# Kernel optimization log

Measured on AMD Instinct MI355X. Metric: run time of the kernel, lower is better.

## Reference

```python
import jax, jax.numpy as jnp
import numpy as np

D_MODEL = 512
NUM_HEADS = 8
D_K = D_MODEL // NUM_HEADS


def setup_inputs() -> dict:
    key = jax.random.key(0)
    k0, k1, k2, k3, k4 = jax.random.split(key, 5)
    s = 1.0 / np.sqrt(D_MODEL)
    return {
        "x": jax.random.normal(k0, (2, 4096, D_MODEL), dtype=jnp.float32),
        "W_q": jax.random.normal(k1, (D_MODEL, D_MODEL), dtype=jnp.float32) * s,
        "W_k": jax.random.normal(k2, (D_MODEL, D_MODEL), dtype=jnp.float32) * s,
        "W_v": jax.random.normal(k3, (D_MODEL, D_MODEL), dtype=jnp.float32) * s,
        "W_o": jax.random.normal(k4, (D_MODEL, D_MODEL), dtype=jnp.float32) * s,
    }


def reference(x, W_q, W_k, W_v, W_o):
    B, S, _ = x.shape
    # project and split heads: (B, H, S, d_k)
    def split(t):
        return t.reshape(B, S, NUM_HEADS, D_K).transpose(0, 2, 1, 3)
    Q = split(x @ W_q)
    K = split(x @ W_k)
    V = split(x @ W_v)
    scale = jnp.sqrt(jnp.asarray(D_K, dtype=x.dtype))
    logits = jnp.einsum('bhqd,bhkd->bhqk', Q, K) / scale
    attn = jax.nn.softmax(logits, axis=-1)  # dropout is identity at inference
    out = jnp.einsum('bhqk,bhkd->bhqd', attn, V)
    concat = out.transpose(0, 2, 1, 3).reshape(B, S, D_MODEL)
    return concat @ W_o
```

## Files before the change

kernel.cpp:

```cpp
#include <hip/hip_runtime.h>
#include <hip/hip_bf16.h>


#define DMODEL 512
#define SEQ    4096
#define NTOK   8192
#define LDQK   1024

using f32x4 = __attribute__((ext_vector_type(4))) float;
using s16x8 = __attribute__((ext_vector_type(8))) short;
using u16x8 = __attribute__((ext_vector_type(8))) unsigned short;

static __device__ __forceinline__ unsigned short f2bf(float f) {
  union { float f; unsigned u; } v; v.f = f;
  unsigned r = v.u + 0x7fff + ((v.u >> 16) & 1);
  return (unsigned short)(r >> 16);
}

static __device__ __forceinline__ unsigned pack_bf2(float lo, float hi) {
  __hip_bfloat162 t = __float22bfloat162_rn(make_float2(lo, hi));
  union { __hip_bfloat162 b; unsigned u; } c; c.b = t; return c.u;
}

__global__ void cast_x_kernel(const float* __restrict__ x,
                              unsigned short* __restrict__ xb, int n4) {
  int i = blockIdx.x * blockDim.x + threadIdx.x;
  if (i >= n4) return;
  float4 v = ((const float4*)x)[i];
  ushort4 o;
  o.x = f2bf(v.x); o.y = f2bf(v.y); o.z = f2bf(v.z); o.w = f2bf(v.w);
  ((ushort4*)xb)[i] = o;
}

__global__ void wtrans4_kernel(const float* __restrict__ Wq,
                               const float* __restrict__ Wk,
                               const float* __restrict__ Wv,
                               const float* __restrict__ Wo,
                               unsigned short* __restrict__ Wall, float c2) {
  int y = blockIdx.y;
  int idx = blockIdx.x * 256 + threadIdx.x;
  const float* W = (y == 0) ? Wq : (y == 1) ? Wk : (y == 2) ? Wv : Wo;
  float scale = (y == 0) ? c2 : 1.0f;
  int k = idx & 511, n = idx >> 9;
  Wall[y * 262144 + idx] = f2bf(W[k * 512 + n] * scale);
}

__global__ __launch_bounds__(256, 3) void gemm_qkv(
    const unsigned short* __restrict__ xb,
    const unsigned short* __restrict__ Wall,
    unsigned short* __restrict__ QKb,
    unsigned short* __restrict__ Vtb)
{
  __shared__ unsigned short As[128 * 32];
  __shared__ unsigned short Bs[128 * 32];
  const int by = blockIdx.y;
  const bool vmode = (by >= 8);
  const unsigned short* A  = vmode ? (Wall + 2 * 262144) : xb;
  const unsigned short* Bt = vmode ? xb : Wall;
  const size_t bm = vmode ? (size_t)(by - 8) * 128 : (size_t)blockIdx.x * 128;
  const size_t bn = vmode ? (size_t)blockIdx.x * 128 : (size_t)by * 128;
  const int tid  = threadIdx.x;
  const int wave = tid >> 6, lane = tid & 63;
  const int q4 = lane >> 4, ln = lane & 15;
  const int wm = (wave >> 1) * 64, wn = (wave & 1) * 64;
  f32x4 acc[4][4] = {};
  const int srow = wave * 16 + (lane >> 2);
  const int scol = (lane & 3) * 8;

  u16x8 a0 = *(const u16x8*)(A  + (bm + srow)      * 512 + scol);
  u16x8 a1 = *(const u16x8*)(A  + (bm + 64 + srow) * 512 + scol);
  u16x8 b0 = *(const u16x8*)(Bt + (bn + srow)      * 512 + scol);
  u16x8 b1 = *(const u16x8*)(Bt + (bn + 64 + srow) * 512 + scol);

  for (int kt = 0; kt < 512; kt += 32) {
    __syncthreads();
    *(u16x8*)(As + srow * 32 + scol)        = a0;
    *(u16x8*)(As + (64 + srow) * 32 + scol) = a1;
    *(u16x8*)(Bs + srow * 32 + scol)        = b0;
    *(u16x8*)(Bs + (64 + srow) * 32 + scol) = b1;
    __syncthreads();
    if (kt + 32 < 512) {
      a0 = *(const u16x8*)(A  + (bm + srow)      * 512 + kt + 32 + scol);
      a1 = *(const u16x8*)(A  + (bm + 64 + srow) * 512 + kt + 32 + scol);
      b0 = *(const u16x8*)(Bt + (bn + srow)      * 512 + kt + 32 + scol);
      b1 = *(const u16x8*)(Bt + (bn + 64 + srow) * 512 + kt + 32 + scol);
    }
    s16x8 af[4], bfr[4];
#pragma unroll
    for (int i = 0; i < 4; i++)
      af[i] = *(const s16x8*)(As + (wm + i * 16 + ln) * 32 + q4 * 8);
#pragma unroll
    for (int i = 0; i < 4; i++)
      bfr[i] = *(const s16x8*)(Bs + (wn + i * 16 + ln) * 32 + q4 * 8);
#pragma unroll
    for (int mi = 0; mi < 4; mi++)
#pragma unroll
      for (int ni = 0; ni < 4; ni++)
        acc[mi][ni] = __builtin_amdgcn_mfma_f32_16x16x32_bf16(
            af[mi], bfr[ni], acc[mi][ni], 0, 0, 0);
  }
#pragma unroll
  for (int mi = 0; mi < 4; mi++)
#pragma unroll
    for (int r = 0; r < 4; ++r) {
      size_t row = bm + wm + mi * 16 + q4 * 4 + r;
#pragma unroll
      for (int ni = 0; ni < 4; ni++) {
        size_t col = bn + wn + ni * 16 + ln;
        unsigned short hv = f2bf(acc[mi][ni][r]);
        if (!vmode) {
          QKb[row * 1024 + col] = hv;
        } else {
          int b = (int)(col >> 12), s = (int)(col & 4095);
          int sp = (s & ~63) | (s & 32) | (((s >> 2) & 3) << 3) |
                   (((s >> 4) & 1) << 2) | (s & 3);
          Vtb[(size_t)b * 2097152 + row * 4096 + sp] = hv;
        }
      }
    }
}

__global__ __launch_bounds__(256, 2) void attn_kernel(
    const unsigned short* __restrict__ QK,
    const unsigned short* __restrict__ Vt,
    unsigned short* __restrict__ Oc)
{
  const int qt = blockIdx.x, h = blockIdx.y, b = blockIdx.z;
  const int tid = threadIdx.x, wave = tid >> 6, lane = tid & 63;
  const int q4 = lane >> 4, ln = lane & 15;
  __shared__ unsigned short Ks[64 * 72];
  __shared__ unsigned short Vs[64 * 72];
  const size_t rowbase = (size_t)b * SEQ;
  const size_t qrow0   = (size_t)qt * 128 + wave * 32;
  const unsigned short* Kp  = QK + rowbase * LDQK + 512 + h * 64;
  const unsigned short* VTp = Vt + ((size_t)(b * 8 + h) * 64) * SEQ;

  s16x8 qf[2][2];
#pragma unroll
  for (int mf = 0; mf < 2; ++mf) {
    const unsigned short* q = QK + (rowbase + qrow0 + mf * 16 + ln) * LDQK + h * 64;
    qf[mf][0] = *(const s16x8*)(q + q4 * 8);
    qf[mf][1] = *(const s16x8*)(q + 32 + q4 * 8);
  }
  f32x4 o[2][4] = {};
  float lp[2] = {};

  const int srow = tid >> 2;
  const int scol = (tid & 3) * 16;

  const unsigned short* kgp = Kp  + (size_t)srow * LDQK + scol;
  const unsigned short* vgp = VTp + (size_t)srow * SEQ  + scol;
  u16x8 kr  = *(const u16x8*)kgp;
  u16x8 kr2 = *(const u16x8*)(kgp + 8);
  u16x8 vr  = *(const u16x8*)vgp;
  u16x8 vr2 = *(const u16x8*)(vgp + 8);

  for (int t = 0; t < SEQ / 64; ++t) {
    __syncthreads();
    *(u16x8*)(Ks + srow * 72 + scol)     = kr;
    *(u16x8*)(Ks + srow * 72 + scol + 8) = kr2;
    *(u16x8*)(Vs + srow * 72 + scol)     = vr;
    *(u16x8*)(Vs + srow * 72 + scol + 8) = vr2;
    __syncthreads();
    if (t + 1 < SEQ / 64) {
      kgp += (size_t)64 * LDQK;
      vgp += 64;
      kr  = *(const u16x8*)kgp;
      kr2 = *(const u16x8*)(kgp + 8);
      vr  = *(const u16x8*)vgp;
      vr2 = *(const u16x8*)(vgp + 8);
    }
    f32x4 s4[2][4] = {};
#pragma unroll
    for (int ni = 0; ni < 4; ni++) {
      const unsigned short* kb = Ks + (ni * 16 + ln) * 72 + q4 * 8;
      s16x8 kf0 = *(const s16x8*)kb;
      s16x8 kf1 = *(const s16x8*)(kb + 32);
#pragma unroll
      for (int mf = 0; mf < 2; ++mf) {
        s4[mf][ni] = __builtin_amdgcn_mfma_f32_16x16x32_bf16(kf0, qf[mf][0], s4[mf][ni], 0, 0, 0);
        s4[mf][ni] = __builtin_amdgcn_mfma_f32_16x16x32_bf16(kf1, qf[mf][1], s4[mf][ni], 0, 0, 0);
      }
    }
    s16x8 pf[2][2];
#pragma unroll
    for (int mf = 0; mf < 2; ++mf) {
      float e[4][4];
      float ls = 0.f;
#pragma unroll
      for (int ni = 0; ni < 4; ni++)
#pragma unroll
        for (int r = 0; r < 4; ++r) {
          e[ni][r] = __builtin_amdgcn_exp2f(s4[mf][ni][r]);
          ls += e[ni][r];
        }
      lp[mf] += ls;
#pragma unroll
      for (int ks = 0; ks < 2; ++ks) {
        union { s16x8 v; unsigned u[4]; } pu;
        pu.u[0] = pack_bf2(e[2 * ks][0],     e[2 * ks][1]);
        pu.u[1] = pack_bf2(e[2 * ks][2],     e[2 * ks][3]);
        pu.u[2] = pack_bf2(e[2 * ks + 1][0], e[2 * ks + 1][1]);
        pu.u[3] = pack_bf2(e[2 * ks + 1][2], e[2 * ks + 1][3]);
        pf[mf][ks] = pu.v;
      }
    }
#pragma unroll
    for (int ks = 0; ks < 2; ++ks)
#pragma unroll
      for (int ni = 0; ni < 4; ni++) {
        s16x8 vf = *(const s16x8*)(Vs + (ni * 16 + ln) * 72 + ks * 32 + q4 * 8);
#pragma unroll
        for (int mf = 0; mf < 2; ++mf)
          o[mf][ni] = __builtin_amdgcn_mfma_f32_16x16x32_bf16(pf[mf][ks], vf, o[mf][ni], 0, 0, 0);
      }
  }
#pragma unroll
  for (int mf = 0; mf < 2; ++mf) {
    float l = lp[mf];
    l += __shfl_xor(l, 16, 64);
    l += __shfl_xor(l, 32, 64);
    lp[mf] = l;
  }
#pragma unroll
  for (int mf = 0; mf < 2; ++mf)
#pragma unroll
    for (int r = 0; r < 4; ++r) {
      float lv = __shfl(lp[mf], q4 * 4 + r, 64);
      float inv = 1.0f / lv;
      size_t row = rowbase + qrow0 + mf * 16 + q4 * 4 + r;
#pragma unroll
      for (int ni = 0; ni < 4; ni++)
        Oc[row * DMODEL + h * 64 + ni * 16 + ln] = f2bf(o[mf][ni][r] * inv);
    }
}

__global__ __launch_bounds__(256, 3) void gemm_out(
    const unsigned short* __restrict__ A,
    const unsigned short* __restrict__ Bt,
    float* __restrict__ C)
{
  __shared__ unsigned short As[128 * 32];
  __shared__ unsigned short Bs[64 * 32];
  const int tid  = threadIdx.x;
  const int wave = tid >> 6, lane = tid & 63;
  const int q4 = lane >> 4, ln = lane & 15;
  const size_t bm = (size_t)blockIdx.x * 128;
  const size_t bn = (size_t)blockIdx.y * 64;
  const int wm = (wave >> 1) * 64, wn = (wave & 1) * 32;
  f32x4 acc[4][2] = {};
  const int srow = wave * 16 + (lane >> 2);
  const int scol = (lane & 3) * 8;

  u16x8 a0 = *(const u16x8*)(A  + (bm + srow)      * 512 + scol);
  u16x8 a1 = *(const u16x8*)(A  + (bm + 64 + srow) * 512 + scol);
  u16x8 b0 = *(const u16x8*)(Bt + (bn + srow)      * 512 + scol);

  for (int kt = 0; kt < 512; kt += 32) {
    __syncthreads();
    *(u16x8*)(As + srow * 32 + scol)        = a0;
    *(u16x8*)(As + (64 + srow) * 32 + scol) = a1;
    *(u16x8*)(Bs + srow * 32 + scol)        = b0;
    __syncthreads();
    if (kt + 32 < 512) {
      a0 = *(const u16x8*)(A  + (bm + srow)      * 512 + kt + 32 + scol);
      a1 = *(const u16x8*)(A  + (bm + 64 + srow) * 512 + kt + 32 + scol);
      b0 = *(const u16x8*)(Bt + (bn + srow)      * 512 + kt + 32 + scol);
    }
    s16x8 af[4], bfr[2];
#pragma unroll
    for (int i = 0; i < 4; i++)
      af[i] = *(const s16x8*)(As + (wm + i * 16 + ln) * 32 + q4 * 8);
#pragma unroll
    for (int i = 0; i < 2; i++)
      bfr[i] = *(const s16x8*)(Bs + (wn + i * 16 + ln) * 32 + q4 * 8);
#pragma unroll
    for (int mi = 0; mi < 4; mi++)
#pragma unroll
      for (int ni = 0; ni < 2; ni++)
        acc[mi][ni] = __builtin_amdgcn_mfma_f32_16x16x32_bf16(
            af[mi], bfr[ni], acc[mi][ni], 0, 0, 0);
  }
#pragma unroll
  for (int mi = 0; mi < 4; mi++)
#pragma unroll
    for (int r = 0; r < 4; ++r) {
      size_t row = bm + wm + mi * 16 + q4 * 4 + r;
#pragma unroll
      for (int ni = 0; ni < 2; ni++)
        C[row * 512 + bn + wn + ni * 16 + ln] = acc[mi][ni][r];
    }
}

extern "C" void kernel_launch(void* const* d_in, const int* in_sizes, int n_in,
                              void* d_out, int out_size, void* d_ws, size_t ws_size,
                              hipStream_t stream) {
  const float* x  = (const float*)d_in[0];
  const float* Wq = (const float*)d_in[1];
  const float* Wk = (const float*)d_in[2];
  const float* Wv = (const float*)d_in[3];
  const float* Wo = (const float*)d_in[4];

  char* ws = (char*)d_ws;
  unsigned short* xb   = (unsigned short*)(ws);
  unsigned short* Wall = (unsigned short*)(ws + 8388608);
  unsigned short* QKb  = (unsigned short*)(ws + 10485760);
  unsigned short* Vtb  = (unsigned short*)(ws + 27262976);
  unsigned short* Oc   = (unsigned short*)(ws + 35651584);

  const float C2 = 0.125f * 1.44269504088896f;

  hipLaunchKernelGGL(cast_x_kernel, dim3(NTOK * DMODEL / 4 / 256), dim3(256), 0,
                     stream, x, xb, NTOK * DMODEL / 4);
  hipLaunchKernelGGL(wtrans4_kernel, dim3(1024, 4), dim3(256), 0, stream,
                     Wq, Wk, Wv, Wo, Wall, C2);
  hipLaunchKernelGGL(gemm_qkv, dim3(64, 12), dim3(256), 0, stream,
                     xb, Wall, QKb, Vtb);
  hipLaunchKernelGGL(attn_kernel, dim3(32, 8, 2), dim3(256), 0, stream,
                     QKb, Vtb, Oc);
  hipLaunchKernelGGL(gemm_out, dim3(64, 8), dim3(256), 0, stream,
                     Oc, Wall + 3 * 262144, (float*)d_out);
}
```

Baseline: 206.4 us.

## Use direct global-to-LDS loads in GEMMs and double-buffer attention K/V tiles

The projection and output GEMMs now use global_load_lds to copy tiles straight into shared memory, in place of staging them through registers with manual prefetch. The attention kernel double-buffers its K and V tiles in shared memory, writing the next tile after the compute, and needs one barrier per iteration instead of two. V fragments are also loaded before the softmax. The aim is to cut register pressure and synchronisation while overlapping loads with MFMA work. The risks are that the GEMMs lose their software prefetch, since the loads now wait at the barrier, and that the doubled LDS in attention may lower occupancy.

Result: faster. 195.6 us (-5.2%).

```diff
diff --git a/kernel.cpp b/kernel.cpp
--- a/kernel.cpp
+++ b/kernel.cpp
@@ -20,6 +20,12 @@
 static __device__ __forceinline__ unsigned pack_bf2(float lo, float hi) {
   __hip_bfloat162 t = __float22bfloat162_rn(make_float2(lo, hi));
   union { __hip_bfloat162 b; unsigned u; } c; c.b = t; return c.u;
+}
+
+static __device__ __forceinline__ void gll16(const void* g, void* l) {
+  __builtin_amdgcn_global_load_lds(
+      (const __attribute__((address_space(1))) unsigned int*)g,
+      (__attribute__((address_space(3))) unsigned int*)l, 16, 0, 0);
 }
 
 __global__ void cast_x_kernel(const float* __restrict__ x,
@@ -67,24 +73,22 @@
   const int srow = wave * 16 + (lane >> 2);
   const int scol = (lane & 3) * 8;
 
-  u16x8 a0 = *(const u16x8*)(A  + (bm + srow)      * 512 + scol);
-  u16x8 a1 = *(const u16x8*)(A  + (bm + 64 + srow) * 512 + scol);
-  u16x8 b0 = *(const u16x8*)(Bt + (bn + srow)      * 512 + scol);
-  u16x8 b1 = *(const u16x8*)(Bt + (bn + 64 + srow) * 512 + scol);
+  const unsigned short* Ag  = A  + (bm + srow)      * 512 + scol;
+  const unsigned short* Ag2 = A  + (bm + 64 + srow) * 512 + scol;
+  const unsigned short* Bg  = Bt + (bn + srow)      * 512 + scol;
+  const unsigned short* Bg2 = Bt + (bn + 64 + srow) * 512 + scol;
+  unsigned short* Ad  = As + wave * 512;
+  unsigned short* Ad2 = As + 2048 + wave * 512;
+  unsigned short* Bd  = Bs + wave * 512;
+  unsigned short* Bd2 = Bs + 2048 + wave * 512;
 
   for (int kt = 0; kt < 512; kt += 32) {
     __syncthreads();
-    *(u16x8*)(As + srow * 32 + scol)        = a0;
-    *(u16x8*)(As + (64 + srow) * 32 + scol) = a1;
-    *(u16x8*)(Bs + srow * 32 + scol)        = b0;
-    *(u16x8*)(Bs + (64 + srow) * 32 + scol) = b1;
-    __syncthreads();
-    if (kt + 32 < 512) {
-      a0 = *(const u16x8*)(A  + (bm + srow)      * 512 + kt + 32 + scol);
-      a1 = *(const u16x8*)(A  + (bm + 64 + srow) * 512 + kt + 32 + scol);
-      b0 = *(const u16x8*)(Bt + (bn + srow)      * 512 + kt + 32 + scol);
-      b1 = *(const u16x8*)(Bt + (bn + 64 + srow) * 512 + kt + 32 + scol);
-    }
+    gll16(Ag + kt,  Ad);
+    gll16(Ag2 + kt, Ad2);
+    gll16(Bg + kt,  Bd);
+    gll16(Bg2 + kt, Bd2);
+    __syncthreads();
     s16x8 af[4], bfr[4];
 #pragma unroll
     for (int i = 0; i < 4; i++)
@@ -128,8 +132,8 @@
   const int qt = blockIdx.x, h = blockIdx.y, b = blockIdx.z;
   const int tid = threadIdx.x, wave = tid >> 6, lane = tid & 63;
   const int q4 = lane >> 4, ln = lane & 15;
-  __shared__ unsigned short Ks[64 * 72];
-  __shared__ unsigned short Vs[64 * 72];
+  __shared__ unsigned short Ks[2][64 * 72];
+  __shared__ unsigned short Vs[2][64 * 72];
   const size_t rowbase = (size_t)b * SEQ;
   const size_t qrow0   = (size_t)qt * 128 + wave * 32;
   const unsigned short* Kp  = QK + rowbase * LDQK + 512 + h * 64;
@@ -150,30 +154,31 @@
 
   const unsigned short* kgp = Kp  + (size_t)srow * LDQK + scol;
   const unsigned short* vgp = VTp + (size_t)srow * SEQ  + scol;
+
   u16x8 kr  = *(const u16x8*)kgp;
   u16x8 kr2 = *(const u16x8*)(kgp + 8);
   u16x8 vr  = *(const u16x8*)vgp;
   u16x8 vr2 = *(const u16x8*)(vgp + 8);
+  *(u16x8*)(Ks[0] + srow * 72 + scol)     = kr;
+  *(u16x8*)(Ks[0] + srow * 72 + scol + 8) = kr2;
+  *(u16x8*)(Vs[0] + srow * 72 + scol)     = vr;
+  *(u16x8*)(Vs[0] + srow * 72 + scol + 8) = vr2;
+  kgp += (size_t)64 * LDQK;  vgp += 64;
+  kr  = *(const u16x8*)kgp;
+  kr2 = *(const u16x8*)(kgp + 8);
+  vr  = *(const u16x8*)vgp;
+  vr2 = *(const u16x8*)(vgp + 8);
+  __syncthreads();
 
   for (int t = 0; t < SEQ / 64; ++t) {
-    __syncthreads();
-    *(u16x8*)(Ks + srow * 72 + scol)     = kr;
-    *(u16x8*)(Ks + srow * 72 + scol + 8) = kr2;
-    *(u16x8*)(Vs + srow * 72 + scol)     = vr;
-    *(u16x8*)(Vs + srow * 72 + scol + 8) = vr2;
-    __syncthreads();
-    if (t + 1 < SEQ / 64) {
-      kgp += (size_t)64 * LDQK;
-      vgp += 64;
-      kr  = *(const u16x8*)kgp;
-      kr2 = *(const u16x8*)(kgp + 8);
-      vr  = *(const u16x8*)vgp;
-      vr2 = *(const u16x8*)(vgp + 8);
-    }
+    const int cur = t & 1;
+    const unsigned short* Kc = Ks[cur];
+    const unsigned short* Vc = Vs[cur];
+
     f32x4 s4[2][4] = {};
 #pragma unroll
     for (int ni = 0; ni < 4; ni++) {
-      const unsigned short* kb = Ks + (ni * 16 + ln) * 72 + q4 * 8;
+      const unsigned short* kb = Kc + (ni * 16 + ln) * 72 + q4 * 8;
       s16x8 kf0 = *(const s16x8*)kb;
       s16x8 kf1 = *(const s16x8*)(kb + 32);
 #pragma unroll
@@ -182,6 +187,13 @@
         s4[mf][ni] = __builtin_amdgcn_mfma_f32_16x16x32_bf16(kf1, qf[mf][1], s4[mf][ni], 0, 0, 0);
       }
     }
+    s16x8 vf[2][4];
+#pragma unroll
+    for (int ks = 0; ks < 2; ++ks)
+#pragma unroll
+      for (int ni = 0; ni < 4; ni++)
+        vf[ks][ni] = *(const s16x8*)(Vc + (ni * 16 + ln) * 72 + ks * 32 + q4 * 8);
+
     s16x8 pf[2][2];
 #pragma unroll
     for (int mf = 0; mf < 2; ++mf) {
@@ -208,12 +220,27 @@
 #pragma unroll
     for (int ks = 0; ks < 2; ++ks)
 #pragma unroll
-      for (int ni = 0; ni < 4; ni++) {
-        s16x8 vf = *(const s16x8*)(Vs + (ni * 16 + ln) * 72 + ks * 32 + q4 * 8);
+      for (int ni = 0; ni < 4; ni++)
 #pragma unroll
         for (int mf = 0; mf < 2; ++mf)
-          o[mf][ni] = __builtin_amdgcn_mfma_f32_16x16x32_bf16(pf[mf][ks], vf, o[mf][ni], 0, 0, 0);
+          o[mf][ni] = __builtin_amdgcn_mfma_f32_16x16x32_bf16(pf[mf][ks], vf[ks][ni], o[mf][ni], 0, 0, 0);
+
+    if (t + 1 < SEQ / 64) {
+      unsigned short* Kn = Ks[cur ^ 1];
+      unsigned short* Vn = Vs[cur ^ 1];
+      *(u16x8*)(Kn + srow * 72 + scol)     = kr;
+      *(u16x8*)(Kn + srow * 72 + scol + 8) = kr2;
+      *(u16x8*)(Vn + srow * 72 + scol)     = vr;
+      *(u16x8*)(Vn + srow * 72 + scol + 8) = vr2;
+      if (t + 2 < SEQ / 64) {
+        kgp += (size_t)64 * LDQK;  vgp += 64;
+        kr  = *(const u16x8*)kgp;
+        kr2 = *(const u16x8*)(kgp + 8);
+        vr  = *(const u16x8*)vgp;
+        vr2 = *(const u16x8*)(vgp + 8);
       }
+    }
+    __syncthreads();
   }
 #pragma unroll
   for (int mf = 0; mf < 2; ++mf) {
@@ -252,21 +279,19 @@
   const int srow = wave * 16 + (lane >> 2);
   const int scol = (lane & 3) * 8;
 
-  u16x8 a0 = *(const u16x8*)(A  + (bm + srow)      * 512 + scol);
-  u16x8 a1 = *(const u16x8*)(A  + (bm + 64 + srow) * 512 + scol);
-  u16x8 b0 = *(const u16x8*)(Bt + (bn + srow)      * 512 + scol);
+  const unsigned short* Ag  = A  + (bm + srow)      * 512 + scol;
+  const unsigned short* Ag2 = A  + (bm + 64 + srow) * 512 + scol;
+  const unsigned short* Bg  = Bt + (bn + srow)      * 512 + scol;
+  unsigned short* Ad  = As + wave * 512;
+  unsigned short* Ad2 = As + 2048 + wave * 512;
+  unsigned short* Bd  = Bs + wave * 512;
 
   for (int kt = 0; kt < 512; kt += 32) {
     __syncthreads();
-    *(u16x8*)(As + srow * 32 + scol)        = a0;
-    *(u16x8*)(As + (64 + srow) * 32 + scol) = a1;
-    *(u16x8*)(Bs + srow * 32 + scol)        = b0;
-    __syncthreads();
-    if (kt + 32 < 512) {
-      a0 = *(const u16x8*)(A  + (bm + srow)      * 512 + kt + 32 + scol);
-      a1 = *(const u16x8*)(A  + (bm + 64 + srow) * 512 + kt + 32 + scol);
-      b0 = *(const u16x8*)(Bt + (bn + srow)      * 512 + kt + 32 + scol);
-    }
+    gll16(Ag + kt,  Ad);
+    gll16(Ag2 + kt, Ad2);
+    gll16(Bg + kt,  Bd);
+    __syncthreads();
     s16x8 af[4], bfr[2];
 #pragma unroll
     for (int i = 0; i < 4; i++)
```
